# Optimization experiments

Measured on AMD Instinct MI355X. Metric: run time of the kernel, lower is better.

The kernel has to match this reference:

```python
import jax, jax.numpy as jnp
import numpy as np

N_POINTS = 300000
NUM_CLUSTERS = 64
LATENT_DIM = 32
DET = 1e-16  # matches `det` in update_gamma


def setup_inputs() -> dict:
    key = jax.random.key(0)
    k1, k2, k3 = jax.random.split(key, 3)
    mu_phi = jax.random.normal(k1, (N_POINTS, LATENT_DIM), dtype=jnp.float32)
    # per-node scalar log-variance (encoder's gcn_logstddev has output dim 1)
    log_cov_phi = jax.random.normal(k2, (N_POINTS, 1), dtype=jnp.float32) * 0.1
    pi_k = jnp.ones((NUM_CLUSTERS,), jnp.float32) / NUM_CLUSTERS
    mu_k = jax.random.normal(k3, (NUM_CLUSTERS, LATENT_DIM), dtype=jnp.float32)
    log_cov_k = jnp.full((NUM_CLUSTERS, 1), 0.1, jnp.float32)
    return {"mu_phi": mu_phi, "log_cov_phi": log_cov_phi, "pi_k": pi_k,
            "mu_k": mu_k, "log_cov_k": log_cov_k, "P": LATENT_DIM}


def _sq_dist(a, b):
    # ||a_i - b_k||^2 via expansion; avoids materializing [N,K,P]
    return (jnp.sum(a * a, axis=1)[:, None]
            - 2.0 * (a @ b.T)
            + jnp.sum(b * b, axis=1)[None, :])


def reference(mu_phi, log_cov_phi, pi_k, mu_k, log_cov_k, P):
    Pf = jnp.float32(P)
    lcp = log_cov_phi[:, 0]          # [N]
    lck = log_cov_k[:, 0]            # [K]
    # --- update_gamma: KL[i,k] between q(z_i) and cluster k (isotropic) ---
    sq = _sq_dist(mu_phi, mu_k)      # [N,K]
    inv_cov_k = jnp.exp(-lck)[None, :]
    KL = 0.5 * (Pf * (lck[None, :] - lcp[:, None]) - Pf
                + Pf * jnp.exp(lcp)[:, None] * inv_cov_k
                + sq * inv_cov_k)    # [N,K]
    w = pi_k[None, :] * jnp.exp(-KL)
    gamma = w / jnp.sum(w, axis=1, keepdims=True) + DET  # [N,K]
    # --- update_others: M-step using the new gamma ---
    N_k = jnp.sum(gamma, axis=0)                          # [K]
    pi_new = N_k / jnp.float32(gamma.shape[0])
    mu_new = (gamma.T @ mu_phi) / N_k[:, None]            # [K,P]
    sq2 = _sq_dist(mu_phi, mu_new)                        # [N,K]
    diff = Pf * jnp.exp(lcp)[:, None] + sq2               # [N,K]
    cov_new = jnp.sum(gamma * diff, axis=0) / (Pf * N_k)  # [K]
    log_cov_new = jnp.log(cov_new)[:, None]               # [K,1]
    return gamma, pi_new, mu_new, log_cov_new
```

## Files before the change

### kernel.cpp

```cpp
#include <hip/hip_runtime.h>
#include <math.h>

#define NPTS 300000
#define K 64
#define P 32
#define DETC 1e-16f
#define WS_FLOATS (K + K + K * P)

#define NBLOCKS 1024
#define NTHREADS 256
#define NWAVES (NBLOCKS * (NTHREADS / 64))
#define CHUNK ((NPTS + NWAVES - 1) / NWAVES)

#define DPP_ADD(v, ctrl)                                                     \
    v += __int_as_float(__builtin_amdgcn_update_dpp(                         \
        0, __float_as_int(v), (ctrl), 0xF, 0xF, true))

__device__ __forceinline__ float rl(float x, int lane) {
    return __int_as_float(__builtin_amdgcn_readlane(__float_as_int(x), lane));
}

__global__ __launch_bounds__(NTHREADS, 4) void em_pass(
    const float* __restrict__ mu_phi,
    const float* __restrict__ log_cov_phi,
    const float* __restrict__ pi_k,
    const float* __restrict__ mu_k,
    const float* __restrict__ log_cov_k,
    float* __restrict__ gamma_out,
    float* __restrict__ out_tail,
    float* __restrict__ ws)
{
    const int lane = threadIdx.x & 63;
    const int wave = threadIdx.x >> 6;
    const int gw = __builtin_amdgcn_readfirstlane(blockIdx.x * (NTHREADS / 64) + wave);

    float muk[P];
#pragma unroll
    for (int d = 0; d < P; ++d) muk[d] = mu_k[lane * P + d];
    const float lck  = log_cov_k[lane];
    const float icov = __expf(-lck);
    const float pik  = pi_k[lane];
    float n2k = 0.f;
#pragma unroll
    for (int d = 0; d < P; ++d) n2k = fmaf(muk[d], muk[d], n2k);
    const float Ak    = 0.5f * (32.f * lck - 32.f + icov * n2k) - __logf(pik);
    const float hicov = 0.5f * icov;

    float accN = 0.f, accS = 0.f;
    float accM[P];
#pragma unroll
    for (int d = 0; d < P; ++d) accM[d] = 0.f;

    const int start = gw * CHUNK;
    const int end0  = (start + CHUNK < NPTS) ? (start + CHUNK) : NPTS;

    for (int gb = start; gb < end0; gb += 64) {
        const int cnt = (end0 - gb < 64) ? (end0 - gb) : 64;

        float u_v = 0.f, lcp_v = 0.f;
        const int ip = gb + lane;
        if (lane < cnt) {
            const float4* r4 = reinterpret_cast<const float4*>(mu_phi + (size_t)ip * P);
            float4 a0 = r4[0], a1 = r4[1], a2 = r4[2], a3 = r4[3];
            float4 a4 = r4[4], a5 = r4[5], a6 = r4[6], a7 = r4[7];
            float n2 = 0.f;
#define N2ACC(q) n2 = fmaf(q.x,q.x,n2); n2 = fmaf(q.y,q.y,n2); \
                 n2 = fmaf(q.z,q.z,n2); n2 = fmaf(q.w,q.w,n2)
            N2ACC(a0); N2ACC(a1); N2ACC(a2); N2ACC(a3);
            N2ACC(a4); N2ACC(a5); N2ACC(a6); N2ACC(a7);
#undef N2ACC
            lcp_v = log_cov_phi[ip];
            u_v   = fmaf(32.f, __expf(lcp_v), n2);
        }

#pragma unroll 2
        for (int p = 0; p < cnt; ++p) {
            const int i = gb + p;
            const float u_s    = rl(u_v, p);
            const float base_s = 16.f * rl(lcp_v, p);
            const float* row = mu_phi + (size_t)i * P;

            float dot = 0.f;
#pragma unroll
            for (int d = 0; d < P; ++d) dot = fmaf(row[d], muk[d], dot);

            const float t = fmaf(-hicov, u_s, base_s) - Ak;
            const float w = __expf(fmaf(icov, dot, t));

            float v = w;
            DPP_ADD(v, 0xB1);
            DPP_ADD(v, 0x4E);
            DPP_ADD(v, 0x128);
            DPP_ADD(v, 0x124);
            const float sum = (rl(v, 0) + rl(v, 16)) + (rl(v, 32) + rl(v, 48));

            const float g = fmaf(w, __builtin_amdgcn_rcpf(sum), DETC);
            gamma_out[(size_t)i * K + lane] = g;

            accN += g;
            accS  = fmaf(g, u_s, accS);
#pragma unroll
            for (int d = 0; d < P; ++d) accM[d] = fmaf(g, row[d], accM[d]);
        }
    }

    __shared__ float lN[K], lS[K], lM[K * P];
    for (int idx = threadIdx.x; idx < K; idx += NTHREADS) { lN[idx] = 0.f; lS[idx] = 0.f; }
    for (int idx = threadIdx.x; idx < K * P; idx += NTHREADS) lM[idx] = 0.f;
    __syncthreads();

    atomicAdd(&lN[lane], accN);
    atomicAdd(&lS[lane], accS);
#pragma unroll
    for (int d = 0; d < P; ++d) atomicAdd(&lM[d * K + lane], accM[d]);
    __syncthreads();

    for (int idx = threadIdx.x; idx < K; idx += NTHREADS) {
        atomicAdd(&ws[idx], lN[idx]);
        atomicAdd(&ws[K + idx], lS[idx]);
    }
    for (int idx = threadIdx.x; idx < K * P; idx += NTHREADS)
        atomicAdd(&ws[2 * K + idx], lM[idx]);
    __syncthreads();

    __shared__ int lastf;
    if (threadIdx.x == 0) {
        __threadfence();
        const int c = atomicAdd((int*)(ws + WS_FLOATS), 1);
        lastf = (c == NBLOCKS - 1);
    }
    __syncthreads();
    if (lastf) {
        __threadfence();
        const int k = threadIdx.x;
        if (k < K) {
            const float Nk = __hip_atomic_load(&ws[k],     __ATOMIC_RELAXED, __HIP_MEMORY_SCOPE_AGENT);
            const float S  = __hip_atomic_load(&ws[K + k], __ATOMIC_RELAXED, __HIP_MEMORY_SCOPE_AGENT);
            float* pi_new      = out_tail;
            float* mu_new      = out_tail + K;
            float* log_cov_new = out_tail + K + K * P;

            pi_new[k] = Nk / (float)NPTS;
            const float invN = 1.f / Nk;
            float m2 = 0.f;
#pragma unroll
            for (int d = 0; d < P; ++d) {
                const float md = __hip_atomic_load(&ws[2 * K + d * K + k],
                                                   __ATOMIC_RELAXED, __HIP_MEMORY_SCOPE_AGENT) * invN;
                mu_new[k * P + d] = md;
                m2 = fmaf(md, md, m2);
            }
            const float cov = (S - Nk * m2) / (32.f * Nk);
            log_cov_new[k] = logf(cov);
        }
    }
}

extern "C" void kernel_launch(void* const* d_in, const int* in_sizes, int n_in,
                              void* d_out, int out_size, void* d_ws, size_t ws_size,
                              hipStream_t stream)
{
    const float* mu_phi      = (const float*)d_in[0];
    const float* log_cov_phi = (const float*)d_in[1];
    const float* pi_k        = (const float*)d_in[2];
    const float* mu_k        = (const float*)d_in[3];
    const float* log_cov_k   = (const float*)d_in[4];
    float* out = (float*)d_out;
    float* ws  = (float*)d_ws;

    hipMemsetAsync(ws, 0, (WS_FLOATS + 1) * sizeof(float), stream);
    em_pass<<<NBLOCKS, NTHREADS, 0, stream>>>(mu_phi, log_cov_phi, pi_k, mu_k,
                                              log_cov_k, out,
                                              out + (size_t)NPTS * K, ws);
}
```

Before: 202.0 us.

## Double block count, prescale cluster means, split dot chains, nontemporal gamma stores

Doubles the grid to 2048 blocks so each wave handles at most 64 points (CHUNK becomes 37), which removes the outer chunk loop and raises the number of waves in flight. Cluster means are prescaled by the inverse covariance and the constant terms are folded, which drops a multiply from each point's exponent. The 32-term dot product is split into four independent FMA chains to shorten the dependency chain. Gamma is written with nontemporal stores to keep the streaming output out of the cache. The cost is twice as many blocks doing the shared-memory and global atomic reductions at the end, and a slightly different rounding order.

```diff
diff --git a/kernel.cpp b/kernel.cpp
--- a/kernel.cpp
+++ b/kernel.cpp
@@ -7,7 +7,7 @@
 #define DETC 1e-16f
 #define WS_FLOATS (K + K + K * P)
 
-#define NBLOCKS 1024
+#define NBLOCKS 2048
 #define NTHREADS 256
 #define NWAVES (NBLOCKS * (NTHREADS / 64))
 #define CHUNK ((NPTS + NWAVES - 1) / NWAVES)
@@ -34,17 +34,21 @@
     const int wave = threadIdx.x >> 6;
     const int gw = __builtin_amdgcn_readfirstlane(blockIdx.x * (NTHREADS / 64) + wave);
 
-    float muk[P];
-#pragma unroll
-    for (int d = 0; d < P; ++d) muk[d] = mu_k[lane * P + d];
     const float lck  = log_cov_k[lane];
     const float icov = __expf(-lck);
     const float pik  = pi_k[lane];
+
+    float mk2[P];
     float n2k = 0.f;
 #pragma unroll
-    for (int d = 0; d < P; ++d) n2k = fmaf(muk[d], muk[d], n2k);
-    const float Ak    = 0.5f * (32.f * lck - 32.f + icov * n2k) - __logf(pik);
-    const float hicov = 0.5f * icov;
+    for (int d = 0; d < P; ++d) {
+        const float m = mu_k[lane * P + d];
+        mk2[d] = icov * m;
+        n2k = fmaf(m, m, n2k);
+    }
+    const float Ak     = 0.5f * (32.f * lck - 32.f + icov * n2k) - __logf(pik);
+    const float negAk  = -Ak;
+    const float nhicov = -0.5f * icov;
 
     float accN = 0.f, accS = 0.f;
     float accM[P];
@@ -53,39 +57,50 @@
 
     const int start = gw * CHUNK;
     const int end0  = (start + CHUNK < NPTS) ? (start + CHUNK) : NPTS;
+    const int cnt   = end0 - start;
 
-    for (int gb = start; gb < end0; gb += 64) {
-        const int cnt = (end0 - gb < 64) ? (end0 - gb) : 64;
-
-        float u_v = 0.f, lcp_v = 0.f;
-        const int ip = gb + lane;
+    if (cnt > 0) {
+        float u_v = 0.f, bl_v = 0.f;
         if (lane < cnt) {
-            const float4* r4 = reinterpret_cast<const float4*>(mu_phi + (size_t)ip * P);
-            float4 a0 = r4[0], a1 = r4[1], a2 = r4[2], a3 = r4[3];
-            float4 a4 = r4[4], a5 = r4[5], a6 = r4[6], a7 = r4[7];
+            const float4* r4 =
+                reinterpret_cast<const float4*>(mu_phi + (size_t)(start + lane) * P);
             float n2 = 0.f;
-#define N2ACC(q) n2 = fmaf(q.x,q.x,n2); n2 = fmaf(q.y,q.y,n2); \
-                 n2 = fmaf(q.z,q.z,n2); n2 = fmaf(q.w,q.w,n2)
-            N2ACC(a0); N2ACC(a1); N2ACC(a2); N2ACC(a3);
-            N2ACC(a4); N2ACC(a5); N2ACC(a6); N2ACC(a7);
-#undef N2ACC
-            lcp_v = log_cov_phi[ip];
-            u_v   = fmaf(32.f, __expf(lcp_v), n2);
+#pragma unroll 1
+            for (int q = 0; q < 8; q += 4) {
+                float4 a = r4[q], b = r4[q + 1], c = r4[q + 2], e = r4[q + 3];
+                n2 = fmaf(a.x, a.x, n2); n2 = fmaf(a.y, a.y, n2);
+                n2 = fmaf(a.z, a.z, n2); n2 = fmaf(a.w, a.w, n2);
+                n2 = fmaf(b.x, b.x, n2); n2 = fmaf(b.y, b.y, n2);
+                n2 = fmaf(b.z, b.z, n2); n2 = fmaf(b.w, b.w, n2);
+                n2 = fmaf(c.x, c.x, n2); n2 = fmaf(c.y, c.y, n2);
+                n2 = fmaf(c.z, c.z, n2); n2 = fmaf(c.w, c.w, n2);
+                n2 = fmaf(e.x, e.x, n2); n2 = fmaf(e.y, e.y, n2);
+                n2 = fmaf(e.z, e.z, n2); n2 = fmaf(e.w, e.w, n2);
+            }
+            const float lcp = log_cov_phi[start + lane];
+            u_v  = fmaf(32.f, __expf(lcp), n2);
+            bl_v = 16.f * lcp;
         }
 
 #pragma unroll 2
         for (int p = 0; p < cnt; ++p) {
-            const int i = gb + p;
-            const float u_s    = rl(u_v, p);
-            const float base_s = 16.f * rl(lcp_v, p);
+            const int i = start + p;
+            const float u_s  = rl(u_v, p);
+            const float bl_s = rl(bl_v, p);
             const float* row = mu_phi + (size_t)i * P;
 
-            float dot = 0.f;
+            float d0 = 0.f, d1 = 0.f, d2 = 0.f, d3 = 0.f;
 #pragma unroll
-            for (int d = 0; d < P; ++d) dot = fmaf(row[d], muk[d], dot);
+            for (int d = 0; d < P; d += 4) {
+                d0 = fmaf(row[d + 0], mk2[d + 0], d0);
+                d1 = fmaf(row[d + 1], mk2[d + 1], d1);
+                d2 = fmaf(row[d + 2], mk2[d + 2], d2);
+                d3 = fmaf(row[d + 3], mk2[d + 3], d3);
+            }
+            const float dot = (d0 + d1) + (d2 + d3);
 
-            const float t = fmaf(-hicov, u_s, base_s) - Ak;
-            const float w = __expf(fmaf(icov, dot, t));
+            const float tpart = fmaf(nhicov, u_s, negAk);
+            const float w = __expf((dot + tpart) + bl_s);
 
             float v = w;
             DPP_ADD(v, 0xB1);
@@ -95,7 +110,7 @@
             const float sum = (rl(v, 0) + rl(v, 16)) + (rl(v, 32) + rl(v, 48));
 
             const float g = fmaf(w, __builtin_amdgcn_rcpf(sum), DETC);
-            gamma_out[(size_t)i * K + lane] = g;
+            __builtin_nontemporal_store(g, gamma_out + (size_t)i * K + lane);
 
             accN += g;
             accS  = fmaf(g, u_s, accS);
```

Result: slower. 249.4 us (+23.5%).
